# Kernel tuning notes

Measured on AMD Instinct MI355X. Metric: run time of the kernel, lower is better.

## Reference

```python
import jax, jax.numpy as jnp
import numpy as np

C = 1.0            # PoincareBall curvature
BALL_EPS = 4e-3    # geoopt projx eps for float32
MIN_NORM = 1e-15


def artanh(x):
    x = jnp.clip(x, -1.0 + 1e-7, 1.0 - 1e-7)
    return 0.5 * (jnp.log1p(x) - jnp.log1p(-x))


def project(x):
    # geoopt projx: clip norm to (1 - eps) / sqrt(c)
    norm = jnp.maximum(jnp.linalg.norm(x, axis=-1, keepdims=True), MIN_NORM)
    maxnorm = (1.0 - BALL_EPS) / jnp.sqrt(C)
    return jnp.where(norm > maxnorm, x / norm * maxnorm, x)


def mobius_matvec(M, x):
    # geoopt mobius_matvec on PoincareBall (followed by project)
    sqrt_c = jnp.sqrt(C)
    x_norm = jnp.maximum(jnp.linalg.norm(x, axis=-1, keepdims=True), MIN_NORM)
    mx = x @ M.T
    mx_norm = jnp.maximum(jnp.linalg.norm(mx, axis=-1, keepdims=True), MIN_NORM)
    res = jnp.tanh(mx_norm / x_norm * artanh(sqrt_c * x_norm)) * mx / (mx_norm * sqrt_c)
    zero_mx = jnp.all(mx == 0.0, axis=-1, keepdims=True)
    return project(jnp.where(zero_mx, 0.0, res))


def mobius_add(x, y):
    # geoopt mobius_add on PoincareBall (followed by project)
    x2 = jnp.sum(x * x, axis=-1, keepdims=True)
    y2 = jnp.sum(y * y, axis=-1, keepdims=True)
    xy = jnp.sum(x * y, axis=-1, keepdims=True)
    num = (1.0 + 2.0 * C * xy + C * y2) * x + (1.0 - C * x2) * y
    den = jnp.maximum(1.0 + 2.0 * C * xy + C * C * x2 * y2, MIN_NORM)
    return project(num / den)


def hyp_linear(x, W, b):
    out = mobius_matvec(W, x)
    return mobius_add(out, b)


def hyperbolic_scores(q, k):
    # q, k: [B, H, S, Dh]
    eps = 1e-5
    q_norm_sq = jnp.minimum(jnp.sum(q * q, axis=-1, keepdims=True), 1.0 - eps)  # [B,H,S,1]
    k_norm_sq = jnp.minimum(jnp.sum(k * k, axis=-1, keepdims=True), 1.0 - eps)  # [B,H,S,1]
    qk = jnp.einsum('bhqd,bhkd->bhqk', q, k)
    k_norm_sq_t = jnp.swapaxes(k_norm_sq, -2, -1)                               # [B,H,1,S]
    denom = (1.0 - q_norm_sq) * (1.0 - k_norm_sq_t) + eps
    delta = 2.0 * ((qk - q_norm_sq * k_norm_sq_t) / denom)
    dist_sq = jnp.sqrt(jnp.maximum(delta, eps))
    return -dist_sq


def setup_inputs() -> dict:
    key = jax.random.key(0)
    B, S, E = 4, 2048, 512
    ks = jax.random.split(key, 5)
    x = jax.random.normal(ks[0], (B, S, E), dtype=jnp.float32) * 0.02  # inside unit ball
    bound = float(np.sqrt(6.0 / (E + E)))  # xavier_uniform
    def w(k):
        return jax.random.uniform(k, (E, E), dtype=jnp.float32, minval=-bound, maxval=bound)
    z = jnp.zeros((E,), dtype=jnp.float32)
    return {
        'x': x,
        'Wq': w(ks[1]), 'bq': z,
        'Wk': w(ks[2]), 'bk': z,
        'Wv': w(ks[3]), 'bv': z,
        'Wo': w(ks[4]), 'bo': z,
    }


def reference(x, Wq, bq, Wk, bk, Wv, bv, Wo, bo):
    B, S, E = x.shape
    H = 8
    Dh = E // H
    q = hyp_linear(x, Wq, bq)
    k = hyp_linear(x, Wk, bk)
    v = hyp_linear(x, Wv, bv)
    # [B,S,E] -> [B,H,S,Dh]
    split = lambda t: t.reshape(B, S, H, Dh).transpose(0, 2, 1, 3)
    q, k, v = split(q), split(k), split(v)
    scores = hyperbolic_scores(q, k) / jnp.sqrt(jnp.float32(Dh))
    attn = jax.nn.softmax(scores, axis=-1)
    out = jnp.einsum('bhqk,bhkd->bhqd', attn, v)
    out = out.transpose(0, 2, 1, 3).reshape(B, S, E)
    return hyp_linear(out, Wo, bo)
```

## Files before the change

### kernel.cpp

```cpp
#include <hip/hip_runtime.h>
#include <math.h>

#define B_ 4
#define S_ 2048
#define E_ 512
#define H_ 8
#define Dh_ 64
#define BS_ (B_*S_)
#define MAXN 0.996f

typedef __attribute__((ext_vector_type(8))) short short8;
typedef __attribute__((ext_vector_type(4))) float f32x4;

__device__ __forceinline__ unsigned f2bf(float x) {
  unsigned u = __float_as_uint(x);
  return (u + 0x7fffu + ((u >> 16) & 1u)) >> 16;
}
__device__ __forceinline__ float bf2f(unsigned b) {
  return __uint_as_float(b << 16);
}

__device__ __forceinline__ void gload_lds16(const void* g, void* lds) {
  __builtin_amdgcn_global_load_lds(
      (const __attribute__((address_space(1))) unsigned int*)g,
      (__attribute__((address_space(3))) unsigned int*)lds, 16, 0, 0);
}

__global__ __launch_bounds__(256) void pack_w_kernel(const float* __restrict__ W0,
    const float* __restrict__ W1, const float* __restrict__ W2,
    const float* __restrict__ W3, unsigned short* __restrict__ Wp) {
  const float* W = (blockIdx.y == 0) ? W0 : (blockIdx.y == 1) ? W1
                 : (blockIdx.y == 2) ? W2 : W3;
  unsigned short* dst = Wp + (size_t)blockIdx.y * 262144;
  int l = threadIdx.x & 63, tq = threadIdx.x >> 6;
  int n = blockIdx.x;
  int col = 16*n + (l & 15);
  int k0 = 8 * (l >> 4);
  #pragma unroll
  for (int tt = 0; tt < 4; ++tt) {
    int t = tq*4 + tt;
    const float* wp_ = W + (size_t)col * E_ + 32*t + k0;
    float4 a0 = *(const float4*)wp_, a1 = *(const float4*)(wp_ + 4);
    float av[8] = {a0.x,a0.y,a0.z,a0.w,a1.x,a1.y,a1.z,a1.w};
    short8 hi;
    #pragma unroll
    for (int j = 0; j < 8; ++j) hi[j] = (short)f2bf(av[j]);
    *(short8*)(dst + ((size_t)(t*32 + n))*512 + l*8) = hi;
  }
}

__global__ __launch_bounds__(256, 3) void qkv_linear(const float* __restrict__ X,
    const unsigned short* __restrict__ Wp,
    const float* __restrict__ bq_, const float* __restrict__ bk_,
    const float* __restrict__ bv_,
    unsigned short* __restrict__ Qhi, unsigned short* __restrict__ Khi,
    unsigned short* __restrict__ Vhi,
    float* __restrict__ qn, float* __restrict__ kn) {
  __shared__ float smM[2][4][4][4], smB[2][4][4][4], smb2[4];
  int tid = threadIdx.x;
  int w = tid >> 6, l = tid & 63;
  int l15 = l & 15, g = l >> 4;
  int R = blockIdx.x;
  int mat = blockIdx.y;
  const unsigned short* Wm = Wp + (size_t)mat * 262144;
  const float* bvec = (mat == 0) ? bq_ : (mat == 1) ? bk_ : bv_;
  unsigned short* outHi = (mat == 0) ? Qhi : (mat == 1) ? Khi : Vhi;
  float* normOut = (mat == 0) ? qn : kn;

  f32x4 acc0[8], acc1[8];
  #pragma unroll
  for (int s = 0; s < 8; ++s) {
    acc0[s] = (f32x4){0.f,0.f,0.f,0.f};
    acc1[s] = (f32x4){0.f,0.f,0.f,0.f};
  }
  const float* xrow0 = X + (size_t)(R*32 + l15)*E_ + 8*g;
  const float* xrow1 = xrow0 + (size_t)16*E_;
  const unsigned short* wl = Wm + (size_t)(8*w)*512 + (size_t)l*8;

  float4 p00 = *(const float4*)xrow0, p01 = *(const float4*)(xrow0 + 4);
  float4 p10 = *(const float4*)xrow1, p11 = *(const float4*)(xrow1 + 4);
  float xsq0 = 0.f, xsq1 = 0.f;

  #pragma unroll 1
  for (int t = 0; t < 16; ++t) {
    const unsigned short* wb = wl + (size_t)t*16384;
    short8 b[8];
    #pragma unroll
    for (int s = 0; s < 8; ++s) b[s] = *(const short8*)(wb + s*512);
    float a0v[8] = {p00.x,p00.y,p00.z,p00.w,p01.x,p01.y,p01.z,p01.w};
    float a1v[8] = {p10.x,p10.y,p10.z,p10.w,p11.x,p11.y,p11.z,p11.w};
    short8 ahi0, alo0, ahi1, alo1;
    #pragma unroll
    for (int j = 0; j < 8; ++j) {
      unsigned hb0 = f2bf(a0v[j]);
      ahi0[j] = (short)hb0;
      alo0[j] = (short)f2bf(a0v[j] - bf2f(hb0));
      xsq0 = fmaf(a0v[j], a0v[j], xsq0);
      unsigned hb1 = f2bf(a1v[j]);
      ahi1[j] = (short)hb1;
      alo1[j] = (short)f2bf(a1v[j] - bf2f(hb1));
      xsq1 = fmaf(a1v[j], a1v[j], xsq1);
    }
    if (t < 15) {
      p00 = *(const float4*)(xrow0 + 32*(t+1));
      p01 = *(const float4*)(xrow0 + 32*(t+1) + 4);
      p10 = *(const float4*)(xrow1 + 32*(t+1));
      p11 = *(const float4*)(xrow1 + 32*(t+1) + 4);
    }
    #pragma unroll
    for (int s = 0; s < 8; ++s) {
      acc0[s] = __builtin_amdgcn_mfma_f32_16x16x32_bf16(ahi0, b[s], acc0[s], 0, 0, 0);
      acc0[s] = __builtin_amdgcn_mfma_f32_16x16x32_bf16(alo0, b[s], acc0[s], 0, 0, 0);
      acc1[s] = __builtin_amdgcn_mfma_f32_16x16x32_bf16(ahi1, b[s], acc1[s], 0, 0, 0);
      acc1[s] = __builtin_amdgcn_mfma_f32_16x16x32_bf16(alo1, b[s], acc1[s], 0, 0, 0);
    }
  }

  xsq0 += __shfl_xor(xsq0, 16, 64); xsq0 += __shfl_xor(xsq0, 32, 64);
  xsq1 += __shfl_xor(xsq1, 16, 64); xsq1 += __shfl_xor(xsq1, 32, 64);
  float xnv4[2][4], art4[2][4];
  #pragma unroll
  for (int i = 0; i < 4; ++i) {
    float s20 = __shfl(xsq0, 4*g + i, 64);
    float s21 = __shfl(xsq1, 4*g + i, 64);
    float xn0 = fmaxf(sqrtf(s20), 1e-15f);
    float xn1 = fmaxf(sqrtf(s21), 1e-15f);
    float aa0 = fminf(xn0, 1.f - 1e-7f);
    float aa1 = fminf(xn1, 1.f - 1e-7f);
    xnv4[0][i] = xn0; art4[0][i] = 0.5f * (log1pf(aa0) - log1pf(-aa0));
    xnv4[1][i] = xn1; art4[1][i] = 0.5f * (log1pf(aa1) - log1pf(-aa1));
  }

  float bl[8];
  #pragma unroll
  for (int s = 0; s < 8; ++s) bl[s] = bvec[16*(8*w+s) + l15];
  float m2p[2][4] = {{0.f,0.f,0.f,0.f},{0.f,0.f,0.f,0.f}};
  float mbp[2][4] = {{0.f,0.f,0.f,0.f},{0.f,0.f,0.f,0.f}};
  float b2p = 0.f;
  #pragma unroll
  for (int s = 0; s < 8; ++s) {
    b2p += bl[s]*bl[s];
    #pragma unroll
    for (int i = 0; i < 4; ++i) {
      m2p[0][i] = fmaf(acc0[s][i], acc0[s][i], m2p[0][i]);
      mbp[0][i] = fmaf(acc0[s][i], bl[s], mbp[0][i]);
      m2p[1][i] = fmaf(acc1[s][i], acc1[s][i], m2p[1][i]);
      mbp[1][i] = fmaf(acc1[s][i], bl[s], mbp[1][i]);
    }
  }
  #pragma unroll
  for (int off = 1; off <= 8; off <<= 1) {
    b2p += __shfl_xor(b2p, off, 64);
    #pragma unroll
    for (int rg = 0; rg < 2; ++rg)
      #pragma unroll
      for (int i = 0; i < 4; ++i) {
        m2p[rg][i] += __shfl_xor(m2p[rg][i], off, 64);
        mbp[rg][i] += __shfl_xor(mbp[rg][i], off, 64);
      }
  }
  if (l == 0) smb2[w] = b2p;
  if (l15 == 0) {
    #pragma unroll
    for (int rg = 0; rg < 2; ++rg)
      #pragma unroll
      for (int i = 0; i < 4; ++i) { smM[rg][w][g][i] = m2p[rg][i]; smB[rg][w][g][i] = mbp[rg][i]; }
  }
  __syncthreads();
  float b2 = smb2[0] + smb2[1] + smb2[2] + smb2[3];
  float G[2][4], Hc[2][4];
  #pragma unroll
  for (int rg = 0; rg < 2; ++rg)
    #pragma unroll
    for (int i = 0; i < 4; ++i) {
      float m2 = smM[rg][0][g][i]+smM[rg][1][g][i]+smM[rg][2][g][i]+smM[rg][3][g][i];
      float mb = smB[rg][0][g][i]+smB[rg][1][g][i]+smB[rg][2][g][i]+smB[rg][3][g][i];
      float xn = xnv4[rg][i], art = art4[rg][i];
      float mn = fmaxf(sqrtf(m2), 1e-15f);
      float t = tanhf(mn / xn * art);
      float alpha, rn;
      if (m2 > 0.f) { alpha = t / mn; rn = t; } else { alpha = 0.f; rn = 0.f; }
      if (rn > MAXN) { alpha *= MAXN / rn; rn = MAXN; }
      float x2r = rn * rn;
      float xy = alpha * mb;
      float A  = 1.f + 2.f*xy + b2;
      float Bc = 1.f - x2r;
      float den = fmaxf(1.f + 2.f*xy + x2r*b2, 1e-15f);
      float n2v = (A*A*x2r + 2.f*A*Bc*xy + Bc*Bc*b2) / (den*den);
      float nn = fmaxf(sqrtf(n2v), 1e-15f);
      float sc = (nn > MAXN) ? (MAXN / nn) : 1.f;
      G[rg][i]  = sc * A * alpha / den;
      Hc[rg][i] = sc * Bc / den;
    }

  #pragma unroll
  for (int rg = 0; rg < 2; ++rg) {
    const f32x4* acc = rg ? acc1 : acc0;
    #pragma unroll
    for (int i = 0; i < 4; ++i) {
      int grow = R*32 + rg*16 + 4*g + i;
      int bb = grow >> 11, seq = grow & 2047;
      int tile = seq >> 6;
      float hn0 = 0.f, hn1 = 0.f;
      #pragma unroll
      for (int s = 0; s < 8; ++s) {
        int col = 16*(8*w+s) + l15;
        float v = G[rg][i]*acc[s][i] + Hc[rg][i]*bl[s];
        int h = col >> 6, c = col & 63;
        size_t base;
        if (mat == 2) {
          int kt = (seq >> 5) & 1, gp = (seq >> 3) & 3, jv = seq & 7;
          int dn = c >> 4, lt = (c & 15) | (gp << 4);
          base = ((size_t)((bb*8 + h)*32 + tile))*4096 + (size_t)((kt*4+dn)*64 + lt)*8 + jv;
        } else {
          int nf = (seq >> 4) & 3, lt15 = seq & 15;
          int dt = c >> 5, m = (c >> 3) & 3, j = c & 7;
          base = ((size_t)((bb*8 + h)*32 + tile))*4096 + (size_t)((dt*4+nf)*64 + (lt15|(m<<4)))*8 + j;
        }
        outHi[base] = (unsigned short)f2bf(v);
        if (mat < 2) { if (s < 4) hn0 += v*v; else hn1 += v*v; }
      }
      if (mat < 2) {
        hn0 += __shfl_xor(hn0,1,64); hn0 += __shfl_xor(hn0,2,64);
        hn0 += __shfl_xor(hn0,4,64); hn0 += __shfl_xor(hn0,8,64);
        hn1 += __shfl_xor(hn1,1,64); hn1 += __shfl_xor(hn1,2,64);
        hn1 += __shfl_xor(hn1,4,64); hn1 += __shfl_xor(hn1,8,64);
        if (l15 == 0) {
          normOut[((size_t)(bb*8 + 2*w + 0))*S_ + seq] = fminf(hn0, 1.f - 1e-5f);
          normOut[((size_t)(bb*8 + 2*w + 1))*S_ + seq] = fminf(hn1, 1.f - 1e-5f);
        }
      }
    }
  }
}

__global__ __launch_bounds__(256, 3) void o_linear(const float* __restrict__ X,
    const unsigned short* __restrict__ Wp, const float* __restrict__ bvec,
    float* __restrict__ outF) {
  __shared__ float smM[2][4][4][4], smB[2][4][4][4], smb2[4];
  int tid = threadIdx.x;
  int w = tid >> 6, l = tid & 63;
  int l15 = l & 15, g = l >> 4;
  int R = blockIdx.x;

  f32x4 acc0[8], acc1[8];
  #pragma unroll
  for (int s = 0; s < 8; ++s) {
    acc0[s] = (f32x4){0.f,0.f,0.f,0.f};
    acc1[s] = (f32x4){0.f,0.f,0.f,0.f};
  }
  const float* xrow0 = X + (size_t)(R*32 + l15)*E_ + 8*g;
  const float* xrow1 = xrow0 + (size_t)16*E_;
  const unsigned short* wl = Wp + (size_t)(8*w)*512 + (size_t)l*8;

  float4 p00 = *(const float4*)xrow0, p01 = *(const float4*)(xrow0 + 4);
  float4 p10 = *(const float4*)xrow1, p11 = *(const float4*)(xrow1 + 4);
  float xsq0 = 0.f, xsq1 = 0.f;

  #pragma unroll 1
  for (int t = 0; t < 16; ++t) {
    const unsigned short* wb = wl + (size_t)t*16384;
    short8 b[8];
    #pragma unroll
    for (int s = 0; s < 8; ++s) b[s] = *(const short8*)(wb + s*512);
    float a0v[8] = {p00.x,p00.y,p00.z,p00.w,p01.x,p01.y,p01.z,p01.w};
    float a1v[8] = {p10.x,p10.y,p10.z,p10.w,p11.x,p11.y,p11.z,p11.w};
    short8 ahi0, alo0, ahi1, alo1;
    #pragma unroll
    for (int j = 0; j < 8; ++j) {
      unsigned hb0 = f2bf(a0v[j]);
      ahi0[j] = (short)hb0;
      alo0[j] = (short)f2bf(a0v[j] - bf2f(hb0));
      xsq0 = fmaf(a0v[j], a0v[j], xsq0);
      unsigned hb1 = f2bf(a1v[j]);
      ahi1[j] = (short)hb1;
      alo1[j] = (short)f2bf(a1v[j] - bf2f(hb1));
      xsq1 = fmaf(a1v[j], a1v[j], xsq1);
    }
    if (t < 15) {
      p00 = *(const float4*)(xrow0 + 32*(t+1));
      p01 = *(const float4*)(xrow0 + 32*(t+1) + 4);
      p10 = *(const float4*)(xrow1 + 32*(t+1));
      p11 = *(const float4*)(xrow1 + 32*(t+1) + 4);
    }
    #pragma unroll
    for (int s = 0; s < 8; ++s) {
      acc0[s] = __builtin_amdgcn_mfma_f32_16x16x32_bf16(ahi0, b[s], acc0[s], 0, 0, 0);
      acc0[s] = __builtin_amdgcn_mfma_f32_16x16x32_bf16(alo0, b[s], acc0[s], 0, 0, 0);
      acc1[s] = __builtin_amdgcn_mfma_f32_16x16x32_bf16(ahi1, b[s], acc1[s], 0, 0, 0);
      acc1[s] = __builtin_amdgcn_mfma_f32_16x16x32_bf16(alo1, b[s], acc1[s], 0, 0, 0);
    }
  }

  xsq0 += __shfl_xor(xsq0, 16, 64); xsq0 += __shfl_xor(xsq0, 32, 64);
  xsq1 += __shfl_xor(xsq1, 16, 64); xsq1 += __shfl_xor(xsq1, 32, 64);
  float xnv4[2][4], art4[2][4];
  #pragma unroll
  for (int i = 0; i < 4; ++i) {
    float s20 = __shfl(xsq0, 4*g + i, 64);
    float s21 = __shfl(xsq1, 4*g + i, 64);
    float xn0 = fmaxf(sqrtf(s20), 1e-15f);
    float xn1 = fmaxf(sqrtf(s21), 1e-15f);
    float aa0 = fminf(xn0, 1.f - 1e-7f);
    float aa1 = fminf(xn1, 1.f - 1e-7f);
    xnv4[0][i] = xn0; art4[0][i] = 0.5f * (log1pf(aa0) - log1pf(-aa0));
    xnv4[1][i] = xn1; art4[1][i] = 0.5f * (log1pf(aa1) - log1pf(-aa1));
  }

  float bl[8];
  #pragma unroll
  for (int s = 0; s < 8; ++s) bl[s] = bvec[16*(8*w+s) + l15];
  float m2p[2][4] = {{0.f,0.f,0.f,0.f},{0.f,0.f,0.f,0.f}};
  float mbp[2][4] = {{0.f,0.f,0.f,0.f},{0.f,0.f,0.f,0.f}};
  float b2p = 0.f;
  #pragma unroll
  for (int s = 0; s < 8; ++s) {
    b2p += bl[s]*bl[s];
    #pragma unroll
    for (int i = 0; i < 4; ++i) {
      m2p[0][i] = fmaf(acc0[s][i], acc0[s][i], m2p[0][i]);
      mbp[0][i] = fmaf(acc0[s][i], bl[s], mbp[0][i]);
      m2p[1][i] = fmaf(acc1[s][i], acc1[s][i], m2p[1][i]);
      mbp[1][i] = fmaf(acc1[s][i], bl[s], mbp[1][i]);
    }
  }
  #pragma unroll
  for (int off = 1; off <= 8; off <<= 1) {
    b2p += __shfl_xor(b2p, off, 64);
    #pragma unroll
    for (int rg = 0; rg < 2; ++rg)
      #pragma unroll
      for (int i = 0; i < 4; ++i) {
        m2p[rg][i] += __shfl_xor(m2p[rg][i], off, 64);
        mbp[rg][i] += __shfl_xor(mbp[rg][i], off, 64);
      }
  }
  if (l == 0) smb2[w] = b2p;
  if (l15 == 0) {
    #pragma unroll
    for (int rg = 0; rg < 2; ++rg)
      #pragma unroll
      for (int i = 0; i < 4; ++i) { smM[rg][w][g][i] = m2p[rg][i]; smB[rg][w][g][i] = mbp[rg][i]; }
  }
  __syncthreads();
  float b2 = smb2[0] + smb2[1] + smb2[2] + smb2[3];
  #pragma unroll
  for (int rg = 0; rg < 2; ++rg) {
    const f32x4* acc = rg ? acc1 : acc0;
    #pragma unroll
    for (int i = 0; i < 4; ++i) {
      float m2 = smM[rg][0][g][i]+smM[rg][1][g][i]+smM[rg][2][g][i]+smM[rg][3][g][i];
      float mb = smB[rg][0][g][i]+smB[rg][1][g][i]+smB[rg][2][g][i]+smB[rg][3][g][i];
      float xn = xnv4[rg][i], art = art4[rg][i];
      float mn = fmaxf(sqrtf(m2), 1e-15f);
      float t = tanhf(mn / xn * art);
      float alpha, rn;
      if (m2 > 0.f) { alpha = t / mn; rn = t; } else { alpha = 0.f; rn = 0.f; }
      if (rn > MAXN) { alpha *= MAXN / rn; rn = MAXN; }
      float x2r = rn * rn;
      float xy = alpha * mb;
      float A  = 1.f + 2.f*xy + b2;
      float Bc = 1.f - x2r;
      float den = fmaxf(1.f + 2.f*xy + x2r*b2, 1e-15f);
      float n2v = (A*A*x2r + 2.f*A*Bc*xy + Bc*Bc*b2) / (den*den);
      float nn = fmaxf(sqrtf(n2v), 1e-15f);
      float sc = (nn > MAXN) ? (MAXN / nn) : 1.f;
      float Gv = sc * A * alpha / den;
      float Hv = sc * Bc / den;
      int grow = R*32 + rg*16 + 4*g + i;
      #pragma unroll
      for (int s = 0; s < 8; ++s)
        outF[(size_t)grow*E_ + 16*(8*w+s) + l15] = Gv*acc[s][i] + Hv*bl[s];
    }
  }
}

__global__ __launch_bounds__(256, 4) void attn_kernel(
    const unsigned short* __restrict__ Qhi, const unsigned short* __restrict__ Khi,
    const unsigned short* __restrict__ Vhi,
    const float* __restrict__ qn_arr, const float* __restrict__ kn_arr,
    float* __restrict__ Out) {
  __shared__ __align__(16) unsigned short Kf[4096];
  __shared__ __align__(16) unsigned short Vf[2][4096];
  __shared__ __align__(16) unsigned short Pf[4][1024];

  int tid = threadIdx.x;
  int w = tid >> 6, l = tid & 63;
  int l15 = l & 15, g = l >> 4;

  int bid = blockIdx.x;
  int xcd = bid & 7, idx = bid >> 3;
  int bh = xcd * 4 + (idx >> 5);
  int qblk = idx & 31;
  int b = bh >> 3, h = bh & 7;
  int qb = qblk * 64;

  const unsigned short* qbase = Qhi + ((size_t)(bh*32 + qblk))*4096;
  short8 qhi[2];
  #pragma unroll
  for (int dt = 0; dt < 2; ++dt)
    qhi[dt] = *(const short8*)(qbase + (size_t)((dt*4 + w)*64 + l)*8);
  float qnv[4], qd[4], rq[4];
  #pragma unroll
  for (int i = 0; i < 4; ++i) {
    qnv[i] = qn_arr[(size_t)bh*S_ + qb + 16*w + 4*g + i];
    qd[i] = 1.f - qnv[i];
    rq[i] = __builtin_amdgcn_rcpf(qd[i]);
  }

  f32x4 Oacc[4];
  #pragma unroll
  for (int dn = 0; dn < 4; ++dn) Oacc[dn] = (f32x4){0.f,0.f,0.f,0.f};
  float lp[4] = {0.f,0.f,0.f,0.f};

  const unsigned short* Kbh = Khi + ((size_t)bh*32)*4096;
  const unsigned short* Vbh = Vhi + ((size_t)bh*32)*4096;
  const float* knp = kn_arr + (size_t)bh*S_;

  #pragma unroll
  for (int r = 0; r < 2; ++r) {
    gload_lds16(Kbh + r*2048 + w*512 + l*8, &Kf[r*2048 + w*512]);
    gload_lds16(Vbh + r*2048 + w*512 + l*8, &Vf[0][r*2048 + w*512]);
  }
  asm volatile("s_waitcnt vmcnt(0)" ::: "memory");
  __syncthreads();

  #pragma unroll 1
  for (int tile = 0; tile < 32; ++tile) {
    int cur = tile & 1;
    int kb = tile * 64;
    float knc[4];
    #pragma unroll
    for (int n = 0; n < 4; ++n) knc[n] = knp[kb + 16*n + l15];
    #pragma unroll
    for (int n = 0; n < 4; ++n) {
      f32x4 Cn = (f32x4){0.f,0.f,0.f,0.f};
      #pragma unroll
      for (int dt = 0; dt < 2; ++dt) {
        short8 kfr = *(const short8*)&Kf[((dt*4 + n)*64 + l)*8];
        Cn = __builtin_amdgcn_mfma_f32_16x16x32_bf16(qhi[dt], kfr, Cn, 0, 0, 0);
      }
      float kd = 1.f - knc[n];
      float rkn = __builtin_amdgcn_rcpf(kd);
      int cbase = (n >> 1)*64 + 16*((2*n + (l15 >> 3)) & 3) + 4*g;
      int csb = cbase ^ ((cbase >> 3) & 7);
      int j7 = l15 & 7;
      #pragma unroll
      for (int i = 0; i < 4; ++i) {
        float num = fmaf(-qnv[i], knc[n], Cn[i]);
        float d2 = fmaxf(num * (rq[i]*rkn), 5e-6f);
        float sq = d2 * __builtin_amdgcn_rsqf(d2);
        float p = __builtin_amdgcn_exp2f(-0.25503386f * sq);
        unsigned u = __float_as_uint(p);
        lp[i] += __uint_as_float(u & 0xffff0000u);
        Pf[w][((csb ^ i) << 3) + j7] = (unsigned short)(u >> 16);
      }
    }
    __builtin_amdgcn_s_barrier();
    if (tile < 31) {
      const unsigned short* kp = Kbh + ((size_t)(tile+1))*4096;
      const unsigned short* vp = Vbh + ((size_t)(tile+1))*4096;
      #pragma unroll
      for (int r = 0; r < 2; ++r)
        gload_lds16(kp + r*2048 + w*512 + l*8, &Kf[r*2048 + w*512]);
      #pragma unroll
      for (int r = 0; r < 2; ++r)
        gload_lds16(vp + r*2048 + w*512 + l*8, &Vf[cur^1][r*2048 + w*512]);
    }
    __builtin_amdgcn_sched_barrier(0);
    short8 pa0, pa1;
    { int c = l;       int cs = c ^ ((c >> 3) & 7); pa0 = *(const short8*)&Pf[w][cs*8]; }
    { int c = 64 + l;  int cs = c ^ ((c >> 3) & 7); pa1 = *(const short8*)&Pf[w][cs*8]; }
    #pragma unroll
    for (int dn = 0; dn < 4; ++dn) {
      short8 v0 = *(const short8*)&Vf[cur][((0*4 + dn)*64 + l)*8];
      short8 v1 = *(const short8*)&Vf[cur][((1*4 + dn)*64 + l)*8];
      f32x4 o = Oacc[dn];
      o = __builtin_amdgcn_mfma_f32_16x16x32_bf16(pa0, v0, o, 0, 0, 0);
      o = __builtin_amdgcn_mfma_f32_16x16x32_bf16(pa1, v1, o, 0, 0, 0);
      Oacc[dn] = o;
    }
    asm volatile("s_waitcnt vmcnt(2)" ::: "memory");
    __builtin_amdgcn_s_barrier();
  }

  #pragma unroll
  for (int i = 0; i < 4; ++i) {
    lp[i] += __shfl_xor(lp[i], 1, 64);
    lp[i] += __shfl_xor(lp[i], 2, 64);
    lp[i] += __shfl_xor(lp[i], 4, 64);
    lp[i] += __shfl_xor(lp[i], 8, 64);
    lp[i] = 1.f / lp[i];
  }
  #pragma unroll
  for (int i = 0; i < 4; ++i) {
    size_t orow = (size_t)(b*S_ + qb + 16*w + 4*g + i)*E_ + h*Dh_;
    #pragma unroll
    for (int dn = 0; dn < 4; ++dn)
      Out[orow + 16*dn + l15] = Oacc[dn][i] * lp[i];
  }
}

extern "C" void kernel_launch(void* const* d_in, const int* in_sizes, int n_in,
                              void* d_out, int out_size, void* d_ws, size_t ws_size,
                              hipStream_t stream) {
  const float* x  = (const float*)d_in[0];
  const float* Wq = (const float*)d_in[1];
  const float* bq = (const float*)d_in[2];
  const float* Wk = (const float*)d_in[3];
  const float* bk = (const float*)d_in[4];
  const float* Wv = (const float*)d_in[5];
  const float* bv = (const float*)d_in[6];
  const float* Wo = (const float*)d_in[7];
  const float* bo = (const float*)d_in[8];
  float* out = (float*)d_out;

  char* p = (char*)d_ws;
  unsigned short* Wp  = (unsigned short*)p; p += (size_t)2  << 20;
  unsigned short* Qhi = (unsigned short*)p; p += (size_t)8  << 20;
  unsigned short* Khi = (unsigned short*)p; p += (size_t)8  << 20;
  unsigned short* Vhi = (unsigned short*)p; p += (size_t)8  << 20;
  float* ao   = (float*)p; p += (size_t)16 << 20;
  float* qn   = (float*)p; p += (size_t)B_*H_*S_ * 4;
  float* kn   = (float*)p; p += (size_t)B_*H_*S_ * 4;

  pack_w_kernel<<<dim3(32, 4), dim3(256), 0, stream>>>(Wq, Wk, Wv, Wo, Wp);
  qkv_linear<<<dim3(BS_/32, 3), dim3(256), 0, stream>>>(x, Wp, bq, bk, bv, Qhi, Khi, Vhi, qn, kn);
  attn_kernel<<<dim3(1024), dim3(256), 0, stream>>>(Qhi, Khi, Vhi, qn, kn, ao);
  o_linear<<<dim3(BS_/32), dim3(256), 0, stream>>>(ao, Wp + 3*262144, bo, out);
}
```

Baseline: 160.5 us.

## Double-buffer weight tiles in LDS via async global-to-LDS loads in linear kernels

The QKV and output projection kernels now prefetch the next K-step's bf16 weight tile straight into a per-wave double-buffered LDS region using global_load_lds, then read the current tile from LDS. Previously each iteration loaded weights directly from global into registers. The goal is to overlap weight fetches with the MFMA work and cut register pressure from in-flight loads. In exchange each block uses 64KB of LDS and launch bounds drop to 2 blocks per CU, which lowers occupancy. A full vmcnt(0) wait at the end of every iteration also serialises the prefetch with the X register loads.

```diff
diff --git a/kernel.cpp b/kernel.cpp
--- a/kernel.cpp
+++ b/kernel.cpp
@@ -49,13 +49,14 @@
   }
 }
 
-__global__ __launch_bounds__(256, 3) void qkv_linear(const float* __restrict__ X,
+__global__ __launch_bounds__(256, 2) void qkv_linear(const float* __restrict__ X,
     const unsigned short* __restrict__ Wp,
     const float* __restrict__ bq_, const float* __restrict__ bk_,
     const float* __restrict__ bv_,
     unsigned short* __restrict__ Qhi, unsigned short* __restrict__ Khi,
     unsigned short* __restrict__ Vhi,
     float* __restrict__ qn, float* __restrict__ kn) {
+  __shared__ __align__(16) unsigned short Wl[4][2][4096];
   __shared__ float smM[2][4][4][4], smB[2][4][4][4], smb2[4];
   int tid = threadIdx.x;
   int w = tid >> 6, l = tid & 63;
@@ -77,16 +78,27 @@
   const float* xrow1 = xrow0 + (size_t)16*E_;
   const unsigned short* wl = Wm + (size_t)(8*w)*512 + (size_t)l*8;
 
+  #pragma unroll
+  for (int s = 0; s < 8; ++s)
+    gload_lds16(wl + s*512, &Wl[w][0][s*512]);
   float4 p00 = *(const float4*)xrow0, p01 = *(const float4*)(xrow0 + 4);
   float4 p10 = *(const float4*)xrow1, p11 = *(const float4*)(xrow1 + 4);
   float xsq0 = 0.f, xsq1 = 0.f;
+  asm volatile("s_waitcnt vmcnt(0)" ::: "memory");
 
   #pragma unroll 1
   for (int t = 0; t < 16; ++t) {
-    const unsigned short* wb = wl + (size_t)t*16384;
+    int cur = t & 1;
+    if (t < 15) {
+      const unsigned short* src = wl + (size_t)(t+1)*16384;
+      #pragma unroll
+      for (int s = 0; s < 8; ++s)
+        gload_lds16(src + s*512, &Wl[w][cur^1][s*512]);
+    }
+    __builtin_amdgcn_sched_barrier(0);
     short8 b[8];
     #pragma unroll
-    for (int s = 0; s < 8; ++s) b[s] = *(const short8*)(wb + s*512);
+    for (int s = 0; s < 8; ++s) b[s] = *(const short8*)&Wl[w][cur][s*512 + l*8];
     float a0v[8] = {p00.x,p00.y,p00.z,p00.w,p01.x,p01.y,p01.z,p01.w};
     float a1v[8] = {p10.x,p10.y,p10.z,p10.w,p11.x,p11.y,p11.z,p11.w};
     short8 ahi0, alo0, ahi1, alo1;
@@ -114,6 +126,7 @@
       acc1[s] = __builtin_amdgcn_mfma_f32_16x16x32_bf16(ahi1, b[s], acc1[s], 0, 0, 0);
       acc1[s] = __builtin_amdgcn_mfma_f32_16x16x32_bf16(alo1, b[s], acc1[s], 0, 0, 0);
     }
+    asm volatile("s_waitcnt vmcnt(0)" ::: "memory");
   }
 
   xsq0 += __shfl_xor(xsq0, 16, 64); xsq0 += __shfl_xor(xsq0, 32, 64);
@@ -234,9 +247,10 @@
   }
 }
 
-__global__ __launch_bounds__(256, 3) void o_linear(const float* __restrict__ X,
+__global__ __launch_bounds__(256, 2) void o_linear(const float* __restrict__ X,
     const unsigned short* __restrict__ Wp, const float* __restrict__ bvec,
     float* __restrict__ outF) {
+  __shared__ __align__(16) unsigned short Wl[4][2][4096];
   __shared__ float smM[2][4][4][4], smB[2][4][4][4], smb2[4];
   int tid = threadIdx.x;
   int w = tid >> 6, l = tid & 63;
@@ -253,16 +267,27 @@
   const float* xrow1 = xrow0 + (size_t)16*E_;
   const unsigned short* wl = Wp + (size_t)(8*w)*512 + (size_t)l*8;
 
+  #pragma unroll
+  for (int s = 0; s < 8; ++s)
+    gload_lds16(wl + s*512, &Wl[w][0][s*512]);
   float4 p00 = *(const float4*)xrow0, p01 = *(const float4*)(xrow0 + 4);
   float4 p10 = *(const float4*)xrow1, p11 = *(const float4*)(xrow1 + 4);
   float xsq0 = 0.f, xsq1 = 0.f;
+  asm volatile("s_waitcnt vmcnt(0)" ::: "memory");
 
   #pragma unroll 1
   for (int t = 0; t < 16; ++t) {
-    const unsigned short* wb = wl + (size_t)t*16384;
+    int cur = t & 1;
+    if (t < 15) {
+      const unsigned short* src = wl + (size_t)(t+1)*16384;
+      #pragma unroll
+      for (int s = 0; s < 8; ++s)
+        gload_lds16(src + s*512, &Wl[w][cur^1][s*512]);
+    }
+    __builtin_amdgcn_sched_barrier(0);
     short8 b[8];
     #pragma unroll
-    for (int s = 0; s < 8; ++s) b[s] = *(const short8*)(wb + s*512);
+    for (int s = 0; s < 8; ++s) b[s] = *(const short8*)&Wl[w][cur][s*512 + l*8];
     float a0v[8] = {p00.x,p00.y,p00.z,p00.w,p01.x,p01.y,p01.z,p01.w};
     float a1v[8] = {p10.x,p10.y,p10.z,p10.w,p11.x,p11.y,p11.z,p11.w};
     short8 ahi0, alo0, ahi1, alo1;
@@ -290,6 +315,7 @@
       acc1[s] = __builtin_amdgcn_mfma_f32_16x16x32_bf16(ahi1, b[s], acc1[s], 0, 0, 0);
       acc1[s] = __builtin_amdgcn_mfma_f32_16x16x32_bf16(alo1, b[s], acc1[s], 0, 0, 0);
     }
+    asm volatile("s_waitcnt vmcnt(0)" ::: "memory");
   }
 
   xsq0 += __shfl_xor(xsq0, 16, 64); xsq0 += __shfl_xor(xsq0, 32, 64);
```

Measured after the change: 179.7 us. 1.12x slower.
